# Kernel tuning notes

Measured on AMD Instinct MI355X. Metric: run time of the kernel, lower is better.

Reference implementation:

```python
import jax, jax.numpy as jnp
import numpy as np

L, T, F, DIM = 16, 16384, 2, 3
N_MIN, N_MAX = 16.0, 512.0
N_PTS = 262144
# torch code builds np.int32 primes [1, 2654435761, 805459861]; 2654435761 wraps to -1640531535.
# Since T is a power of two, int32 wraparound multiply/xor followed by nonnegative mod T gives
# bit-identical indices to the int64 torch computation.
PIS = jnp.array([1, -1640531535, 805459861], dtype=jnp.int32)
# corner ordering from get_indices: corner k = a*4+b*2+c with a->dim0, b->dim1, c->dim2
OFFS = jnp.array([[(k >> 2) & 1, (k >> 1) & 1, k & 1] for k in range(8)], dtype=jnp.float32)  # (8,3)


def setup_inputs() -> dict:
    key = jax.random.key(0)
    k1, k2 = jax.random.split(key)
    x = jax.random.uniform(k1, (N_PTS, DIM), dtype=jnp.float32)
    # nn.init.uniform_(weight, a=-1e-4, b=1e-4) for each of L tables of shape (T, F)
    embeddings = jax.random.uniform(k2, (L, T, F), minval=-1e-4, maxval=1e-4, dtype=jnp.float32)
    return {"x": x, "embeddings": embeddings}


def reference(x, embeddings):
    # per-level growth factor b = exp((log Nmax - log Nmin)/L); N_l = Nmin * b**l
    b = jnp.exp((jnp.log(N_MAX) - jnp.log(N_MIN)) / L)
    N_l = N_MIN * b ** jnp.arange(L, dtype=jnp.float32)                      # (L,)
    un_x = x[None, :, :] * N_l[:, None, None]                                # (L,N,3)  (mu=0, sigma=1)
    lo = jnp.floor(un_x)
    hi = jnp.ceil(un_x)
    d = hi - lo                                                              # (L,N,3)
    nz = d != 0
    diff = jnp.where(nz, (un_x - lo) / jnp.where(nz, d, 1.0), 0.0)           # (L,N,3)

    mask = OFFS.astype(bool)[None, None]                                     # (1,1,8,3)
    corners = jnp.where(mask, hi[:, :, None, :], lo[:, :, None, :])          # (L,N,8,3)
    ci = corners.astype(jnp.int32)
    prod = ci * PIS                                                          # (L,N,8,3) wrapping int32 mul
    idx = jnp.mod(prod[..., 0] ^ prod[..., 1] ^ prod[..., 2], T)             # (L,N,8)

    # per-level table gather: (L,T,F)[ (L,N,8) ] -> (L,N,8,F)
    feats = jax.vmap(lambda emb, i: emb[i])(embeddings, idx)

    # trilinear weights: prod over dims of (diff if corner bit else 1-diff)
    w = jnp.prod(jnp.where(mask, diff[:, :, None, :], 1.0 - diff[:, :, None, :]), axis=-1)  # (L,N,8)
    c = jnp.einsum('lnc,lncf->lnf', w, feats)                                # (L,N,F)
    return jnp.transpose(c, (1, 0, 2)).reshape(x.shape[0], L * F)            # (N, L*F)
```

## Files before the change

### kernel.cpp

```cpp
#include <hip/hip_runtime.h>
#include <stdint.h>

constexpr int L_LEVELS = 16;
constexpr int T_SIZE   = 16384;
constexpr int N_PTS    = 262144;

typedef _Float16 h2 __attribute__((ext_vector_type(2)));
typedef _Float16 h8 __attribute__((ext_vector_type(8)));

constexpr uint32_t P1_4 = 2654435761u * 4u;
constexpr uint32_t P2_4 = 805459861u * 4u;
constexpr uint32_t M4   = (T_SIZE - 1) * 4u;

__device__ __forceinline__ h2 lerp2(h2 a, h2 b, h2 t) {
    return a + t * (b - a);
}

template <bool DIRECT>
__global__ __launch_bounds__(512, 4) void hash_encode_lds(
    const float* __restrict__ x,
    const float* __restrict__ emb,
    void* __restrict__ dst_raw)
{
    __shared__ h2 tab[T_SIZE];

    const int l     = blockIdx.x & (L_LEVELS - 1);
    const int chunk = blockIdx.x >> 4;
    const int t     = threadIdx.x;
    const int n0    = chunk * 4096 + t * 8;

    {
        const float4* __restrict__ src =
            reinterpret_cast<const float4*>(emb + (size_t)l * T_SIZE * 2);
        h8* __restrict__ d8 = reinterpret_cast<h8*>(tab);
#pragma unroll
        for (int it = 0; it < 8; ++it) {
            const int i = it * 512 + t;
            float4 a = src[2 * i];
            float4 b = src[2 * i + 1];
            h8 w = { (_Float16)a.x, (_Float16)a.y, (_Float16)a.z, (_Float16)a.w,
                     (_Float16)b.x, (_Float16)b.y, (_Float16)b.z, (_Float16)b.w };
            d8[i] = w;
        }
    }

    union { float4 q[6]; float f[24]; } xs;
    {
        const float4* __restrict__ xv =
            reinterpret_cast<const float4*>(x + (size_t)n0 * 3);
#pragma unroll
        for (int i = 0; i < 6; ++i) xs.q[i] = xv[i];
    }

    __syncthreads();

    const float Nl = 16.0f * exp2f((float)l * 0.3125f);
    const char* __restrict__ tb = reinterpret_cast<const char*>(tab);

    union { h2 r[8]; float4 q[2]; } res;

#pragma unroll
    for (int p = 0; p < 8; ++p) {
        const float u0 = xs.f[3 * p + 0] * Nl;
        const float u1 = xs.f[3 * p + 1] * Nl;
        const float u2 = xs.f[3 * p + 2] * Nl;

        const float fl0 = floorf(u0), fl1 = floorf(u1), fl2 = floorf(u2);
        const float df0 = u0 - fl0, df1 = u1 - fl1, df2 = u2 - fl2;

        const uint32_t q0 = ((uint32_t)(int32_t)fl0) << 2;
        const uint32_t q1 = ((uint32_t)(int32_t)fl1) * P1_4;
        const uint32_t q2 = ((uint32_t)(int32_t)fl2) * P2_4;
        const uint32_t d0 = (q0 ^ (q0 + 4u))   & M4;
        const uint32_t d1 = (q1 ^ (q1 + P1_4)) & M4;
        const uint32_t d2 = (q2 ^ (q2 + P2_4)) & M4;

        uint32_t off = (q0 ^ q1 ^ q2) & M4;

        constexpr int gray[8] = {0, 1, 3, 2, 6, 7, 5, 4};
        h2 f[8];
#pragma unroll
        for (int j = 0; j < 8; ++j) {
            f[gray[j]] = *reinterpret_cast<const h2*>(tb + off);
            if (j < 7) {
                const int tog = gray[j] ^ gray[j + 1];
                off ^= (tog == 4) ? d0 : (tog == 2) ? d1 : d2;
            }
        }

        const _Float16 h0 = (_Float16)df0, h1 = (_Float16)df1, hv2 = (_Float16)df2;
        const h2 t0 = {h0, h0}, t1 = {h1, h1}, t2 = {hv2, hv2};
        h2 e0 = lerp2(f[0], f[1], t2);
        h2 e1 = lerp2(f[2], f[3], t2);
        h2 e2 = lerp2(f[4], f[5], t2);
        h2 e3 = lerp2(f[6], f[7], t2);
        h2 g0 = lerp2(e0, e1, t1);
        h2 g1 = lerp2(e2, e3, t1);
        res.r[p] = lerp2(g0, g1, t0);
    }

    if (DIRECT) {
        float2* out = reinterpret_cast<float2*>(dst_raw);
#pragma unroll
        for (int p = 0; p < 8; ++p)
            out[(size_t)(n0 + p) * L_LEVELS + l] =
                make_float2((float)res.r[p].x, (float)res.r[p].y);
    } else {
        float4* ws4 = reinterpret_cast<float4*>(
            reinterpret_cast<h2*>(dst_raw) + (size_t)l * N_PTS + n0);
        ws4[0] = res.q[0];
        ws4[1] = res.q[1];
    }
}

__global__ __launch_bounds__(256) void transpose_lnf_nlf(
    const h2* __restrict__ ws,
    float2* __restrict__ out)
{
    __shared__ h2 tile[L_LEVELS][257];
    const int t    = threadIdx.x;
    const int base = blockIdx.x * 256;

#pragma unroll
    for (int l = 0; l < L_LEVELS; ++l)
        tile[l][t] = ws[(size_t)l * N_PTS + base + t];
    __syncthreads();

#pragma unroll
    for (int i = 0; i < L_LEVELS; ++i) {
        const int flat = i * 256 + t;
        const int p = flat >> 4;
        const int l = flat & 15;
        h2 v = tile[l][p];
        out[(size_t)base * L_LEVELS + flat] =
            make_float2((float)v.x, (float)v.y);
    }
}

extern "C" void kernel_launch(void* const* d_in, const int* in_sizes, int n_in,
                              void* d_out, int out_size, void* d_ws, size_t ws_size,
                              hipStream_t stream) {
    const float* x   = (const float*)d_in[0];
    const float* emb = (const float*)d_in[1];

    const size_t ws_needed = (size_t)N_PTS * L_LEVELS * sizeof(h2);

    if (ws_size >= ws_needed) {
        hash_encode_lds<false><<<1024, 512, 0, stream>>>(x, emb, d_ws);
        transpose_lnf_nlf<<<N_PTS / 256, 256, 0, stream>>>((const h2*)d_ws,
                                                           (float2*)d_out);
    } else {
        hash_encode_lds<true><<<1024, 512, 0, stream>>>(x, emb, d_out);
    }
}
```

Before: 86.54 us.

## Fuse per-level encoding and transpose into one kernel with double-buffered LDS tables

Replaces the level-major encode kernel and separate transpose with a per-point kernel. Each thread processes all 16 levels for one point and writes its output row directly. A small pre-kernel converts all tables to fp16. Inside the fused kernel, the next level's table is staged through registers into a second LDS buffer while the current level is looked up, which removes the workspace round trip and the transpose pass. In exchange, only 256 blocks of 1024 threads are launched, each using 128KB of LDS, so occupancy is low and there are 15 block-wide barriers per block. The fallback path also now does the final lerp in fp32.

```diff
diff --git a/kernel.cpp b/kernel.cpp
--- a/kernel.cpp
+++ b/kernel.cpp
@@ -16,55 +16,59 @@
     return a + t * (b - a);
 }
 
-template <bool DIRECT>
-__global__ __launch_bounds__(512, 4) void hash_encode_lds(
+__global__ __launch_bounds__(256) void cvt_tables(
+    const float* __restrict__ emb, h2* __restrict__ tbl)
+{
+    const int i = blockIdx.x * 256 + threadIdx.x;
+    const float4* __restrict__ s = reinterpret_cast<const float4*>(emb);
+    float4 a = s[2 * i];
+    float4 b = s[2 * i + 1];
+    h8 w = { (_Float16)a.x, (_Float16)a.y, (_Float16)a.z, (_Float16)a.w,
+             (_Float16)b.x, (_Float16)b.y, (_Float16)b.z, (_Float16)b.w };
+    reinterpret_cast<h8*>(tbl)[i] = w;
+}
+
+__global__ __launch_bounds__(1024, 4) void hash_encode_fused(
     const float* __restrict__ x,
-    const float* __restrict__ emb,
-    void* __restrict__ dst_raw)
+    const h2*    __restrict__ tbl,
+    float4*      __restrict__ out)
 {
-    __shared__ h2 tab[T_SIZE];
-
-    const int l     = blockIdx.x & (L_LEVELS - 1);
-    const int chunk = blockIdx.x >> 4;
-    const int t     = threadIdx.x;
-    const int n0    = chunk * 4096 + t * 8;
+    __shared__ h2 tab[2][T_SIZE];
+
+    const int t = threadIdx.x;
+    const int n = blockIdx.x * 1024 + t;
+
+    const float x0 = x[3 * n + 0];
+    const float x1 = x[3 * n + 1];
+    const float x2 = x[3 * n + 2];
 
     {
-        const float4* __restrict__ src =
-            reinterpret_cast<const float4*>(emb + (size_t)l * T_SIZE * 2);
-        h8* __restrict__ d8 = reinterpret_cast<h8*>(tab);
-#pragma unroll
-        for (int it = 0; it < 8; ++it) {
-            const int i = it * 512 + t;
-            float4 a = src[2 * i];
-            float4 b = src[2 * i + 1];
-            h8 w = { (_Float16)a.x, (_Float16)a.y, (_Float16)a.z, (_Float16)a.w,
-                     (_Float16)b.x, (_Float16)b.y, (_Float16)b.z, (_Float16)b.w };
-            d8[i] = w;
-        }
-    }
-
-    union { float4 q[6]; float f[24]; } xs;
-    {
-        const float4* __restrict__ xv =
-            reinterpret_cast<const float4*>(x + (size_t)n0 * 3);
-#pragma unroll
-        for (int i = 0; i < 6; ++i) xs.q[i] = xv[i];
-    }
-
+        const h8* __restrict__ s = reinterpret_cast<const h8*>(tbl);
+        h8* __restrict__ d = reinterpret_cast<h8*>(tab[0]);
+#pragma unroll
+        for (int r = 0; r < 4; ++r) d[r * 1024 + t] = s[r * 1024 + t];
+    }
     __syncthreads();
 
-    const float Nl = 16.0f * exp2f((float)l * 0.3125f);
-    const char* __restrict__ tb = reinterpret_cast<const char*>(tab);
-
-    union { h2 r[8]; float4 q[2]; } res;
-
-#pragma unroll
-    for (int p = 0; p < 8; ++p) {
-        const float u0 = xs.f[3 * p + 0] * Nl;
-        const float u1 = xs.f[3 * p + 1] * Nl;
-        const float u2 = xs.f[3 * p + 2] * Nl;
-
+    h2 res[L_LEVELS];
+
+#pragma unroll
+    for (int l = 0; l < L_LEVELS; ++l) {
+        h8 stg0, stg1, stg2, stg3;
+        if (l < L_LEVELS - 1) {
+            const h8* __restrict__ s =
+                reinterpret_cast<const h8*>(tbl + (size_t)(l + 1) * T_SIZE);
+            stg0 = s[0 * 1024 + t];
+            stg1 = s[1 * 1024 + t];
+            stg2 = s[2 * 1024 + t];
+            stg3 = s[3 * 1024 + t];
+        }
+
+        const float Nl = 16.0f * exp2f((float)l * 0.3125f);
+        const char* __restrict__ tb =
+            reinterpret_cast<const char*>(tab[l & 1]);
+
+        const float u0 = x0 * Nl, u1 = x1 * Nl, u2 = x2 * Nl;
         const float fl0 = floorf(u0), fl1 = floorf(u1), fl2 = floorf(u2);
         const float df0 = u0 - fl0, df1 = u1 - fl1, df2 = u2 - fl2;
 
@@ -96,44 +100,105 @@
         h2 e3 = lerp2(f[6], f[7], t2);
         h2 g0 = lerp2(e0, e1, t1);
         h2 g1 = lerp2(e2, e3, t1);
-        res.r[p] = lerp2(g0, g1, t0);
-    }
-
-    if (DIRECT) {
-        float2* out = reinterpret_cast<float2*>(dst_raw);
-#pragma unroll
-        for (int p = 0; p < 8; ++p)
-            out[(size_t)(n0 + p) * L_LEVELS + l] =
-                make_float2((float)res.r[p].x, (float)res.r[p].y);
-    } else {
-        float4* ws4 = reinterpret_cast<float4*>(
-            reinterpret_cast<h2*>(dst_raw) + (size_t)l * N_PTS + n0);
-        ws4[0] = res.q[0];
-        ws4[1] = res.q[1];
-    }
-}
-
-__global__ __launch_bounds__(256) void transpose_lnf_nlf(
-    const h2* __restrict__ ws,
-    float2* __restrict__ out)
+        res[l] = lerp2(g0, g1, t0);
+
+        if (l < L_LEVELS - 1) {
+            h8* __restrict__ d = reinterpret_cast<h8*>(tab[(l + 1) & 1]);
+            d[0 * 1024 + t] = stg0;
+            d[1 * 1024 + t] = stg1;
+            d[2 * 1024 + t] = stg2;
+            d[3 * 1024 + t] = stg3;
+            __syncthreads();
+        }
+    }
+
+    float4* __restrict__ o = out + (size_t)n * 8;
+#pragma unroll
+    for (int i = 0; i < 8; ++i)
+        o[i] = make_float4((float)res[2 * i].x,     (float)res[2 * i].y,
+                           (float)res[2 * i + 1].x, (float)res[2 * i + 1].y);
+}
+
+__global__ __launch_bounds__(512, 4) void hash_encode_lds_direct(
+    const float* __restrict__ x,
+    const float* __restrict__ emb,
+    float2* __restrict__ dst)
 {
-    __shared__ h2 tile[L_LEVELS][257];
-    const int t    = threadIdx.x;
-    const int base = blockIdx.x * 256;
-
-#pragma unroll
-    for (int l = 0; l < L_LEVELS; ++l)
-        tile[l][t] = ws[(size_t)l * N_PTS + base + t];
+    __shared__ h2 tab[T_SIZE];
+
+    const int l     = blockIdx.x & (L_LEVELS - 1);
+    const int chunk = blockIdx.x >> 4;
+    const int t     = threadIdx.x;
+    const int n0    = chunk * 4096 + t * 8;
+
+    {
+        const float4* __restrict__ src =
+            reinterpret_cast<const float4*>(emb + (size_t)l * T_SIZE * 2);
+        h8* __restrict__ d8 = reinterpret_cast<h8*>(tab);
+#pragma unroll
+        for (int it = 0; it < 8; ++it) {
+            const int i = it * 512 + t;
+            float4 a = src[2 * i];
+            float4 b = src[2 * i + 1];
+            h8 w = { (_Float16)a.x, (_Float16)a.y, (_Float16)a.z, (_Float16)a.w,
+                     (_Float16)b.x, (_Float16)b.y, (_Float16)b.z, (_Float16)b.w };
+            d8[i] = w;
+        }
+    }
+
+    union { float4 q[6]; float f[24]; } xs;
+    {
+        const float4* __restrict__ xv =
+            reinterpret_cast<const float4*>(x + (size_t)n0 * 3);
+#pragma unroll
+        for (int i = 0; i < 6; ++i) xs.q[i] = xv[i];
+    }
+
     __syncthreads();
 
-#pragma unroll
-    for (int i = 0; i < L_LEVELS; ++i) {
-        const int flat = i * 256 + t;
-        const int p = flat >> 4;
-        const int l = flat & 15;
-        h2 v = tile[l][p];
-        out[(size_t)base * L_LEVELS + flat] =
-            make_float2((float)v.x, (float)v.y);
+    const float Nl = 16.0f * exp2f((float)l * 0.3125f);
+    const char* __restrict__ tb = reinterpret_cast<const char*>(tab);
+
+#pragma unroll
+    for (int p = 0; p < 8; ++p) {
+        const float u0 = xs.f[3 * p + 0] * Nl;
+        const float u1 = xs.f[3 * p + 1] * Nl;
+        const float u2 = xs.f[3 * p + 2] * Nl;
+
+        const float fl0 = floorf(u0), fl1 = floorf(u1), fl2 = floorf(u2);
+        const float df0 = u0 - fl0, df1 = u1 - fl1, df2 = u2 - fl2;
+
+        const uint32_t q0 = ((uint32_t)(int32_t)fl0) << 2;
+        const uint32_t q1 = ((uint32_t)(int32_t)fl1) * P1_4;
+        const uint32_t q2 = ((uint32_t)(int32_t)fl2) * P2_4;
+        const uint32_t d0 = (q0 ^ (q0 + 4u))   & M4;
+        const uint32_t d1 = (q1 ^ (q1 + P1_4)) & M4;
+        const uint32_t d2 = (q2 ^ (q2 + P2_4)) & M4;
+
+        uint32_t off = (q0 ^ q1 ^ q2) & M4;
+
+        constexpr int gray[8] = {0, 1, 3, 2, 6, 7, 5, 4};
+        h2 f[8];
+#pragma unroll
+        for (int j = 0; j < 8; ++j) {
+            f[gray[j]] = *reinterpret_cast<const h2*>(tb + off);
+            if (j < 7) {
+                const int tog = gray[j] ^ gray[j + 1];
+                off ^= (tog == 4) ? d0 : (tog == 2) ? d1 : d2;
+            }
+        }
+
+        const _Float16 h0 = (_Float16)df0, h1 = (_Float16)df1, hv2 = (_Float16)df2;
+        const h2 t0 = {h0, h0}, t1 = {h1, h1}, t2 = {hv2, hv2};
+        h2 e0 = lerp2(f[0], f[1], t2);
+        h2 e1 = lerp2(f[2], f[3], t2);
+        h2 e2 = lerp2(f[4], f[5], t2);
+        h2 e3 = lerp2(f[6], f[7], t2);
+        h2 g0 = lerp2(e0, e1, t1);
+        h2 g1 = lerp2(e2, e3, t1);
+        dst[(size_t)(n0 + p) * L_LEVELS + l] =
+            make_float2((float)g0.x + (float)t0.x * ((float)g1.x - (float)g0.x),
+                        (float)g0.y + (float)t0.y * ((float)g1.y - (float)g0.y));
     }
 }
 
@@ -143,13 +208,14 @@
     const float* x   = (const float*)d_in[0];
     const float* emb = (const float*)d_in[1];
 
-    const size_t ws_needed = (size_t)N_PTS * L_LEVELS * sizeof(h2);
-
-    if (ws_size >= ws_needed) {
-        hash_encode_lds<false><<<1024, 512, 0, stream>>>(x, emb, d_ws);
-        transpose_lnf_nlf<<<N_PTS / 256, 256, 0, stream>>>((const h2*)d_ws,
-                                                           (float2*)d_out);
+    const size_t tbl_bytes = (size_t)L_LEVELS * T_SIZE * sizeof(h2);
+
+    if (ws_size >= tbl_bytes) {
+        cvt_tables<<<256, 256, 0, stream>>>(emb, (h2*)d_ws);
+        hash_encode_fused<<<256, 1024, 0, stream>>>(x, (const h2*)d_ws,
+                                                    (float4*)d_out);
     } else {
-        hash_encode_lds<true><<<1024, 512, 0, stream>>>(x, emb, d_out);
-    }
-}
+        hash_encode_lds_direct<<<1024, 512, 0, stream>>>(x, emb,
+                                                         (float2*)d_out);
+    }
+}
```

Result: slower. 110.9 us (+28.2%).

## Drop workspace transpose and write output directly with level-grouped block order

Applied to the files above, without the earlier changes.

Removes the second transpose kernel and the fp16 workspace round-trip, so the encoder writes float2 results straight into the (N, L*F) output. Block indices are remapped so that 8 consecutive blocks cover 8 chunks at the same level, and consecutive levels of a chunk run close together in time, which helps strided output writes merge in L2. The point loop is also restructured to process two points at a time, issuing 16 LDS gathers before the lerps to raise memory-level parallelism. The cost is strided 8-byte global stores in place of coalesced ones, plus some extra register pressure.

```diff
diff --git a/kernel.cpp b/kernel.cpp
--- a/kernel.cpp
+++ b/kernel.cpp
@@ -16,16 +16,16 @@
     return a + t * (b - a);
 }
 
-template <bool DIRECT>
-__global__ __launch_bounds__(512, 4) void hash_encode_lds(
+__global__ __launch_bounds__(512, 4) void hash_encode_direct(
     const float* __restrict__ x,
     const float* __restrict__ emb,
-    void* __restrict__ dst_raw)
+    float2*      __restrict__ out)
 {
     __shared__ h2 tab[T_SIZE];
 
-    const int l     = blockIdx.x & (L_LEVELS - 1);
-    const int chunk = blockIdx.x >> 4;
+    const int bid   = blockIdx.x;
+    const int l     = (bid >> 3) & 15;
+    const int chunk = (bid & 7) + ((bid >> 7) << 3);
     const int t     = threadIdx.x;
     const int n0    = chunk * 4096 + t * 8;
 
@@ -51,89 +51,67 @@
 #pragma unroll
         for (int i = 0; i < 6; ++i) xs.q[i] = xv[i];
     }
-
     __syncthreads();
 
     const float Nl = 16.0f * exp2f((float)l * 0.3125f);
     const char* __restrict__ tb = reinterpret_cast<const char*>(tab);
 
-    union { h2 r[8]; float4 q[2]; } res;
+#pragma unroll
+    for (int pp = 0; pp < 8; pp += 2) {
+        uint32_t off[2], dd0[2], dd1[2], dd2[2];
+        h2 tt0[2], tt1[2], tt2[2];
+#pragma unroll
+        for (int k = 0; k < 2; ++k) {
+            const int p = pp + k;
+            const float u0 = xs.f[3 * p + 0] * Nl;
+            const float u1 = xs.f[3 * p + 1] * Nl;
+            const float u2 = xs.f[3 * p + 2] * Nl;
 
+            const float fl0 = floorf(u0), fl1 = floorf(u1), fl2 = floorf(u2);
+            const float df0 = u0 - fl0, df1 = u1 - fl1, df2 = u2 - fl2;
+
+            const uint32_t q0 = ((uint32_t)(int32_t)fl0) << 2;
+            const uint32_t q1 = ((uint32_t)(int32_t)fl1) * P1_4;
+            const uint32_t q2 = ((uint32_t)(int32_t)fl2) * P2_4;
+            dd0[k] = (q0 ^ (q0 + 4u))   & M4;
+            dd1[k] = (q1 ^ (q1 + P1_4)) & M4;
+            dd2[k] = (q2 ^ (q2 + P2_4)) & M4;
+            off[k] = (q0 ^ q1 ^ q2) & M4;
+
+            const _Float16 h0 = (_Float16)df0, h1 = (_Float16)df1,
+                           hv2 = (_Float16)df2;
+            tt0[k] = h2{h0, h0};
+            tt1[k] = h2{h1, h1};
+            tt2[k] = h2{hv2, hv2};
+        }
+
+        h2 f[2][8];
 #pragma unroll
-    for (int p = 0; p < 8; ++p) {
-        const float u0 = xs.f[3 * p + 0] * Nl;
-        const float u1 = xs.f[3 * p + 1] * Nl;
-        const float u2 = xs.f[3 * p + 2] * Nl;
-
-        const float fl0 = floorf(u0), fl1 = floorf(u1), fl2 = floorf(u2);
-        const float df0 = u0 - fl0, df1 = u1 - fl1, df2 = u2 - fl2;
-
-        const uint32_t q0 = ((uint32_t)(int32_t)fl0) << 2;
-        const uint32_t q1 = ((uint32_t)(int32_t)fl1) * P1_4;
-        const uint32_t q2 = ((uint32_t)(int32_t)fl2) * P2_4;
-        const uint32_t d0 = (q0 ^ (q0 + 4u))   & M4;
-        const uint32_t d1 = (q1 ^ (q1 + P1_4)) & M4;
-        const uint32_t d2 = (q2 ^ (q2 + P2_4)) & M4;
-
-        uint32_t off = (q0 ^ q1 ^ q2) & M4;
-
-        constexpr int gray[8] = {0, 1, 3, 2, 6, 7, 5, 4};
-        h2 f[8];
+        for (int k = 0; k < 2; ++k) {
+            constexpr int gray[8] = {0, 1, 3, 2, 6, 7, 5, 4};
+            uint32_t o = off[k];
 #pragma unroll
-        for (int j = 0; j < 8; ++j) {
-            f[gray[j]] = *reinterpret_cast<const h2*>(tb + off);
-            if (j < 7) {
-                const int tog = gray[j] ^ gray[j + 1];
-                off ^= (tog == 4) ? d0 : (tog == 2) ? d1 : d2;
+            for (int j = 0; j < 8; ++j) {
+                f[k][gray[j]] = *reinterpret_cast<const h2*>(tb + o);
+                if (j < 7) {
+                    const int tog = gray[j] ^ gray[j + 1];
+                    o ^= (tog == 4) ? dd0[k] : (tog == 2) ? dd1[k] : dd2[k];
+                }
             }
         }
 
-        const _Float16 h0 = (_Float16)df0, h1 = (_Float16)df1, hv2 = (_Float16)df2;
-        const h2 t0 = {h0, h0}, t1 = {h1, h1}, t2 = {hv2, hv2};
-        h2 e0 = lerp2(f[0], f[1], t2);
-        h2 e1 = lerp2(f[2], f[3], t2);
-        h2 e2 = lerp2(f[4], f[5], t2);
-        h2 e3 = lerp2(f[6], f[7], t2);
-        h2 g0 = lerp2(e0, e1, t1);
-        h2 g1 = lerp2(e2, e3, t1);
-        res.r[p] = lerp2(g0, g1, t0);
-    }
-
-    if (DIRECT) {
-        float2* out = reinterpret_cast<float2*>(dst_raw);
 #pragma unroll
-        for (int p = 0; p < 8; ++p)
-            out[(size_t)(n0 + p) * L_LEVELS + l] =
-                make_float2((float)res.r[p].x, (float)res.r[p].y);
-    } else {
-        float4* ws4 = reinterpret_cast<float4*>(
-            reinterpret_cast<h2*>(dst_raw) + (size_t)l * N_PTS + n0);
-        ws4[0] = res.q[0];
-        ws4[1] = res.q[1];
-    }
-}
-
-__global__ __launch_bounds__(256) void transpose_lnf_nlf(
-    const h2* __restrict__ ws,
-    float2* __restrict__ out)
-{
-    __shared__ h2 tile[L_LEVELS][257];
-    const int t    = threadIdx.x;
-    const int base = blockIdx.x * 256;
-
-#pragma unroll
-    for (int l = 0; l < L_LEVELS; ++l)
-        tile[l][t] = ws[(size_t)l * N_PTS + base + t];
-    __syncthreads();
-
-#pragma unroll
-    for (int i = 0; i < L_LEVELS; ++i) {
-        const int flat = i * 256 + t;
-        const int p = flat >> 4;
-        const int l = flat & 15;
-        h2 v = tile[l][p];
-        out[(size_t)base * L_LEVELS + flat] =
-            make_float2((float)v.x, (float)v.y);
+        for (int k = 0; k < 2; ++k) {
+            h2 e0 = lerp2(f[k][0], f[k][1], tt2[k]);
+            h2 e1 = lerp2(f[k][2], f[k][3], tt2[k]);
+            h2 e2 = lerp2(f[k][4], f[k][5], tt2[k]);
+            h2 e3 = lerp2(f[k][6], f[k][7], tt2[k]);
+            h2 g0 = lerp2(e0, e1, tt1[k]);
+            h2 g1 = lerp2(e2, e3, tt1[k]);
+            h2 r  = lerp2(g0, g1, tt0[k]);
+            out[(size_t)(n0 + pp + k) * L_LEVELS + l] =
+                make_float2((float)r.x, (float)r.y);
+        }
     }
 }
 
@@ -142,14 +120,7 @@
                               hipStream_t stream) {
     const float* x   = (const float*)d_in[0];
     const float* emb = (const float*)d_in[1];
+    (void)d_ws; (void)ws_size;
 
-    const size_t ws_needed = (size_t)N_PTS * L_LEVELS * sizeof(h2);
-
-    if (ws_size >= ws_needed) {
-        hash_encode_lds<false><<<1024, 512, 0, stream>>>(x, emb, d_ws);
-        transpose_lnf_nlf<<<N_PTS / 256, 256, 0, stream>>>((const h2*)d_ws,
-                                                           (float2*)d_out);
-    } else {
-        hash_encode_lds<true><<<1024, 512, 0, stream>>>(x, emb, d_out);
-    }
+    hash_encode_direct<<<1024, 512, 0, stream>>>(x, emb, (float2*)d_out);
 }
```

Measured after the change: 92.00 us. 6.3% more time.
